# Kernel tuning notes

Measured on AMD Instinct MI355X. Metric: run time of the kernel, lower is better.

## Reference

```python
import jax, jax.numpy as jnp
import numpy as np

B, C, N = 4, 256, 4096
BN_EPS = 1e-5


def setup_inputs() -> dict:
    key = jax.random.key(0)
    ks = jax.random.split(key, 8)
    Cq = C // 4
    return {
        "x": jax.random.normal(ks[0], (B, C, N), dtype=jnp.float32),
        # q_conv and k_conv share weights (self.q_conv.weight = self.k_conv.weight)
        "w_qk": jax.random.normal(ks[1], (Cq, C), dtype=jnp.float32) * 0.05,
        "w_v": jax.random.normal(ks[2], (C, C), dtype=jnp.float32) * 0.05,
        "b_v": jax.random.normal(ks[3], (C,), dtype=jnp.float32) * 0.05,
        # LBR: Conv1d(C,C,1) + BN1d (inference stats) + ReLU
        "w_lbr": jax.random.normal(ks[4], (C, C), dtype=jnp.float32) * 0.05,
        "b_lbr": jax.random.normal(ks[5], (C,), dtype=jnp.float32) * 0.05,
        "bn_gamma": jnp.ones((C,), dtype=jnp.float32),
        "bn_beta": jnp.zeros((C,), dtype=jnp.float32),
        "bn_mean": jax.random.normal(ks[6], (C,), dtype=jnp.float32) * 0.05,
        "bn_var": jax.random.uniform(ks[7], (C,), dtype=jnp.float32, minval=0.5, maxval=1.5),
    }


def reference(x, w_qk, w_v, b_v, w_lbr, b_lbr, bn_gamma, bn_beta, bn_mean, bn_var):
    # x: [B, C, N]
    chans = x.shape[1]
    # conv1x1 Q/K (shared weight, no bias), V (with bias)
    x_q = jnp.einsum('qc,bcn->bnq', w_qk, x)          # [B, N, C/4]
    x_k = jnp.einsum('qc,bcm->bqm', w_qk, x)          # [B, C/4, N]
    x_v = jnp.einsum('oc,bcn->bon', w_v, x) + b_v[None, :, None]  # [B, C, N]
    # energy: [B, N_query, N_key]
    energy = jnp.einsum('bnq,bqm->bnm', x_q, x_k)
    # 'SL' normalization: scale by C**-0.5, softmax over dim=-2 (query axis)
    energy = energy * (chans ** -0.5)
    attention = jax.nn.softmax(energy, axis=-2)        # [B, N, N]
    # x_r[b,c,m] = sum_n x_v[b,c,n] * attention[b,n,m]
    x_r = jnp.einsum('bcn,bnm->bcm', x_v, attention)   # [B, C, N]
    # offset residual
    x_r = x - x_r
    # LBR: conv1x1 -> BN (inference) -> ReLU
    h = jnp.einsum('oc,bcn->bon', w_lbr, x_r) + b_lbr[None, :, None]
    inv_std = jax.lax.rsqrt(bn_var + BN_EPS)
    h = (h - bn_mean[None, :, None]) * (inv_std * bn_gamma)[None, :, None] + bn_beta[None, :, None]
    h = jax.nn.relu(h)
    return x + h
```

## Files before the change

### kernel.cpp

```cpp
#include <hip/hip_runtime.h>
#include <hip/hip_bf16.h>
#include <stdint.h>
#include <math.h>

#define Bq 4
#define Cc 256
#define Nn 4096
#define CQ 64
#define QKSCALE 0.30028060219661246f

typedef short s16x4 __attribute__((ext_vector_type(4)));
typedef short s16x8 __attribute__((ext_vector_type(8)));
typedef unsigned int u32x4 __attribute__((ext_vector_type(4)));
typedef float f32x16 __attribute__((ext_vector_type(16)));

#define MFMA32(a,b,c) __builtin_amdgcn_mfma_f32_32x32x16_bf16((a),(b),(c),0,0,0)

static __device__ __forceinline__ unsigned short f2b(float f) {
  unsigned int u = __float_as_uint(f);
  u += 0x7FFFu + ((u >> 16) & 1u);
  return (unsigned short)(u >> 16);
}

static __device__ __forceinline__ unsigned short f2bh(float f) {
  __hip_bfloat16 h = __float2bfloat16(f);
  return __builtin_bit_cast(unsigned short, h);
}

static __device__ __forceinline__ float b2f(unsigned short u) {
  return __uint_as_float(((unsigned int)u) << 16);
}

static __device__ __forceinline__ float fexp2(float x) {
#if __has_builtin(__builtin_amdgcn_exp2f)
  return __builtin_amdgcn_exp2f(x);
#else
  return exp2f(x);
#endif
}

static __device__ __forceinline__ f32x16 fz16() {
  f32x16 z;
#pragma unroll
  for (int i = 0; i < 16; i++) z[i] = 0.0f;
  return z;
}

static __device__ __forceinline__ float sum16(f32x16 E) {
  return (((E[0] + E[1]) + (E[2] + E[3])) + ((E[4] + E[5]) + (E[6] + E[7]))) +
         (((E[8] + E[9]) + (E[10] + E[11])) + ((E[12] + E[13]) + (E[14] + E[15])));
}

__global__ __launch_bounds__(256) void k_prep(
    const float* __restrict__ wqk, const float* __restrict__ wv,
    const float* __restrict__ wlbr, const float* __restrict__ blbr,
    const float* __restrict__ gamma, const float* __restrict__ beta,
    const float* __restrict__ mean, const float* __restrict__ var,
    unsigned short* __restrict__ Wcat, float* __restrict__ sd,
    unsigned int* __restrict__ mxb) {
  int bx = blockIdx.x, t = threadIdx.x;
  if (bx < 576) {
    float v;
    if (bx < 64) v = wqk[bx * 256 + t] * QKSCALE;
    else if (bx < 320) v = wv[(bx - 64) * 256 + t];
    else v = wlbr[(bx - 320) * 256 + t];
    Wcat[bx * 256 + t] = f2b(v);
  } else {
    float s = gamma[t] * rsqrtf(var[t] + 1e-5f);
    sd[t] = s;
    sd[256 + t] = beta[t] + (blbr[t] - mean[t]) * s;
    if (t < 4) mxb[t] = 0u;
  }
}

__global__ __launch_bounds__(640) void k_proj(const float* __restrict__ x,
                                              const unsigned short* __restrict__ Wcat,
                                              const float* __restrict__ bv,
                                              unsigned short* __restrict__ qkT,
                                              unsigned short* __restrict__ Vf,
                                              unsigned short* __restrict__ xT) {
  __shared__ unsigned short xs[32 * 264];
  int bx = blockIdx.x;
  int b = bx >> 7;
  int ntile = bx & 127;
  int n0 = ntile * 32;
  int t = threadIdx.x;
  const float* xb = x + (size_t)b * Cc * Nn;
  for (int u = t; u < 1024; u += 640) {
    int c = u >> 2, j = (u & 3) * 8;
    const float* src = &xb[(size_t)c * Nn + n0 + j];
    float4 v0 = *(const float4*)src;
    float4 v1 = *(const float4*)(src + 4);
    xs[(j + 0) * 264 + c] = f2b(v0.x);
    xs[(j + 1) * 264 + c] = f2b(v0.y);
    xs[(j + 2) * 264 + c] = f2b(v0.z);
    xs[(j + 3) * 264 + c] = f2b(v0.w);
    xs[(j + 4) * 264 + c] = f2b(v1.x);
    xs[(j + 5) * 264 + c] = f2b(v1.y);
    xs[(j + 6) * 264 + c] = f2b(v1.z);
    xs[(j + 7) * 264 + c] = f2b(v1.w);
  }
  int w = t >> 6, a = t & 31, g = (t >> 5) & 1;
  bool isqk = (w >= 8);
  int row0 = isqk ? (w - 8) * 32 : 64 + w * 32;
  s16x8 wf[16];
#pragma unroll
  for (int kc = 0; kc < 16; kc++)
    wf[kc] = *(const s16x8*)&Wcat[(size_t)(row0 + a) * 256 + kc * 16 + 8 * g];
  __syncthreads();
  unsigned short* xTb = xT + ((size_t)b * Nn + n0) * Cc;
  for (int u = t; u < 1024; u += 640) {
    int row = u >> 5, ch = u & 31;
    *(s16x8*)&xTb[(size_t)row * Cc + ch * 8] = *(const s16x8*)&xs[row * 264 + ch * 8];
  }
  f32x16 acc = fz16();
#pragma unroll
  for (int kc = 0; kc < 16; kc++) {
    s16x8 xf = *(const s16x8*)&xs[a * 264 + kc * 16 + 8 * g];
    acc = MFMA32(xf, wf[kc], acc);
  }
  if (isqk) {
    unsigned short* dst = qkT + ((size_t)b * Nn + n0) * CQ;
    int q0 = row0;
#pragma unroll
    for (int r = 0; r < 16; r++) {
      int n = (r & 3) + 8 * (r >> 2) + 4 * g;
      dst[(size_t)n * CQ + q0 + a] = f2b(acc[r]);
    }
  } else {
    int c0 = row0 - 64;
    float bvv = bv[c0 + a];
    s16x8 vlo, vhi;
#pragma unroll
    for (int r = 0; r < 8; r++) {
      vlo[r] = (short)f2b(acc[r] + bvv);
      vhi[r] = (short)f2b(acc[8 + r] + bvv);
    }
    unsigned short* dstF =
        Vf + ((size_t)(b * 128 + ntile) * 4 + g) * 2048 + (size_t)(c0 + a) * 8;
    *(s16x8*)dstF = vlo;
    *(s16x8*)(dstF + 4096) = vhi;
  }
}

__global__ __launch_bounds__(256) void k_norm(const unsigned short* __restrict__ qkT,
                                              float* __restrict__ nrm,
                                              unsigned int* __restrict__ mxb) {
  int idx = blockIdx.x * 256 + threadIdx.x;
  const unsigned short* row = qkT + (size_t)idx * CQ;
  float s = 0.0f;
#pragma unroll
  for (int k = 0; k < 8; k++) {
    s16x8 v = *(const s16x8*)&row[k * 8];
#pragma unroll
    for (int j = 0; j < 8; j++) {
      float f = b2f((unsigned short)v[j]);
      s += f * f;
    }
  }
  float nr = sqrtf(s);
  nrm[idx] = nr;
  float m = nr;
#pragma unroll
  for (int off = 1; off < 64; off <<= 1) m = fmaxf(m, __shfl_xor(m, off, 64));
  __shared__ float wm[4];
  if ((threadIdx.x & 63) == 0) wm[threadIdx.x >> 6] = m;
  __syncthreads();
  if (threadIdx.x == 0) {
    float mm = fmaxf(fmaxf(wm[0], wm[1]), fmaxf(wm[2], wm[3]));
    atomicMax(mxb + (idx >> 12), __float_as_uint(mm));
  }
}

__global__ __launch_bounds__(512, 2) void k_attn(const unsigned short* __restrict__ qkT,
                                                 const unsigned short* __restrict__ Vf,
                                                 const float* __restrict__ nrm,
                                                 const unsigned int* __restrict__ mxb,
                                                 unsigned short* __restrict__ xT) {
  __shared__ __align__(16) float Pf[4 * 128 * 33];
  __shared__ float Ls[4 * 64];
  int bx = blockIdx.x;
  int id = ((bx & 7) << 5) | (bx >> 3);
  int b = id >> 6;
  int m0 = (id & 63) * 64;
  int t = threadIdx.x;
  int w = t >> 6, a = t & 31, g = (t >> 5) & 1;
  int cs = w >> 2, ns = w & 3;
  const unsigned short* qkTb = qkT + (size_t)b * Nn * CQ;
  s16x8 Bq0[4], Bq1[4];
#pragma unroll
  for (int kc = 0; kc < 4; kc++) {
    Bq0[kc] = *(const s16x8*)&qkTb[(size_t)(m0 + a) * CQ + kc * 16 + 8 * g];
    Bq1[kc] = *(const s16x8*)&qkTb[(size_t)(m0 + 32 + a) * CQ + kc * 16 + 8 * g];
  }
  float mxf = __uint_as_float(mxb[b]);
  float Mh0 = nrm[(size_t)b * Nn + m0 + a] * mxf + 0.01f;
  float Mh1 = nrm[(size_t)b * Nn + m0 + 32 + a] * mxf + 0.01f;
  const unsigned short* Vc = Vf + (size_t)b * 1048576 + (size_t)g * 2048 +
                             (size_t)(cs * 128 + a) * 8;
  f32x16 acc[8];
#pragma unroll
  for (int i = 0; i < 8; i++) acc[i] = fz16();
  float Lp0 = 0.0f, Lp1 = 0.0f;
  s16x8 qf[4];
#pragma unroll
  for (int kc = 0; kc < 4; kc++)
    qf[kc] = *(const s16x8*)&qkTb[(size_t)(ns * 32 + a) * CQ + kc * 16 + 8 * g];
#pragma unroll 1
  for (int nt = ns; nt < 128; nt += 4) {
    const unsigned short* Vt = Vc + (size_t)nt * 8192;
    f32x16 E0 = fz16(), E1 = fz16();
#pragma unroll
    for (int kc = 0; kc < 4; kc++) E0 = MFMA32(qf[kc], Bq0[kc], E0);
    s16x8 va0, va1, va2, va3;
    va0 = *(const s16x8*)&Vt[0];
    va1 = *(const s16x8*)&Vt[4096];
    va2 = *(const s16x8*)&Vt[256];
    va3 = *(const s16x8*)&Vt[4096 + 256];
#pragma unroll
    for (int kc = 0; kc < 4; kc++) E1 = MFMA32(qf[kc], Bq1[kc], E1);
    int ntn = (nt + 4) & 127;
#pragma unroll
    for (int kc = 0; kc < 4; kc++)
      qf[kc] = *(const s16x8*)&qkTb[(size_t)(ntn * 32 + a) * CQ + kc * 16 + 8 * g];
#pragma unroll
    for (int r = 0; r < 16; r++) E0[r] = fexp2(E0[r] - Mh0);
    Lp0 += sum16(E0);
    s16x8 p00, p01;
#pragma unroll
    for (int j = 0; j < 8; j++) {
      p00[j] = (short)f2bh(E0[j]);
      p01[j] = (short)f2bh(E0[8 + j]);
    }
#pragma unroll
    for (int r = 0; r < 16; r++) E1[r] = fexp2(E1[r] - Mh1);
    Lp1 += sum16(E1);
    s16x8 p10, p11;
#pragma unroll
    for (int j = 0; j < 8; j++) {
      p10[j] = (short)f2bh(E1[j]);
      p11[j] = (short)f2bh(E1[8 + j]);
    }
    acc[0] = MFMA32(p00, va0, acc[0]);
    acc[4] = MFMA32(p10, va0, acc[4]);
    acc[1] = MFMA32(p00, va2, acc[1]);
    acc[5] = MFMA32(p10, va2, acc[5]);
    acc[0] = MFMA32(p01, va1, acc[0]);
    acc[4] = MFMA32(p11, va1, acc[4]);
    acc[1] = MFMA32(p01, va3, acc[1]);
    acc[5] = MFMA32(p11, va3, acc[5]);
    s16x8 vb0, vb1, vb2, vb3;
    vb0 = *(const s16x8*)&Vt[512];
    vb1 = *(const s16x8*)&Vt[4096 + 512];
    vb2 = *(const s16x8*)&Vt[768];
    vb3 = *(const s16x8*)&Vt[4096 + 768];
    acc[2] = MFMA32(p00, vb0, acc[2]);
    acc[6] = MFMA32(p10, vb0, acc[6]);
    acc[3] = MFMA32(p00, vb2, acc[3]);
    acc[7] = MFMA32(p10, vb2, acc[7]);
    acc[2] = MFMA32(p01, vb1, acc[2]);
    acc[6] = MFMA32(p11, vb1, acc[6]);
    acc[3] = MFMA32(p01, vb3, acc[3]);
    acc[7] = MFMA32(p11, vb3, acc[7]);
  }
  float Lw0 = Lp0 + __shfl_xor(Lp0, 32, 64);
  float Lw1 = Lp1 + __shfl_xor(Lp1, 32, 64);
  if (cs == 0 && (t & 63) < 32) {
    Ls[ns * 64 + a] = Lw0;
    Ls[ns * 64 + 32 + a] = Lw1;
  }
  unsigned short* xTb = xT + ((size_t)b * Nn + m0) * Cc;
#pragma unroll
  for (int q = 0; q < 4; q++) {
    int qmt = q >> 1, qcs = q & 1;
    __syncthreads();
    if (cs == qcs) {
#pragma unroll
      for (int ct = 0; ct < 4; ct++) {
        float* dst = &Pf[(size_t)(ns * 128 + ct * 32 + a) * 33];
        f32x16 A = acc[qmt * 4 + ct];
#pragma unroll
        for (int r = 0; r < 16; r++) {
          int mrow = (r & 3) + 8 * (r >> 2) + 4 * g;
          dst[mrow] = A[r];
        }
      }
    }
    __syncthreads();
    int m = t & 31, c8 = t >> 5;
    float rL = 1.0f / (((Ls[qmt * 32 + m] + Ls[64 + qmt * 32 + m]) +
                        (Ls[128 + qmt * 32 + m] + Ls[192 + qmt * 32 + m])));
    unsigned short* xrow = &xTb[(size_t)(qmt * 32 + m) * Cc + qcs * 128 + c8 * 8];
    s16x8 xv = *(const s16x8*)xrow;
#pragma unroll
    for (int j = 0; j < 8; j++) {
      int cl = c8 * 8 + j;
      float s = ((Pf[(0 * 128 + cl) * 33 + m] + Pf[(1 * 128 + cl) * 33 + m]) +
                 (Pf[(2 * 128 + cl) * 33 + m] + Pf[(3 * 128 + cl) * 33 + m]));
      xv[j] = (short)f2b(b2f((unsigned short)xv[j]) - s * rL);
    }
    *(s16x8*)xrow = xv;
  }
}

__global__ __launch_bounds__(512) void k_lbr(const unsigned short* __restrict__ xrT,
                                             const unsigned short* __restrict__ Wcat,
                                             const float* __restrict__ sd,
                                             const float* __restrict__ x,
                                             float* __restrict__ out) {
  __shared__ unsigned short xs[32 * 264];
  __shared__ float sL[256], dL[256];
  int bx = blockIdx.x;
  int b = bx >> 7;
  int n0 = (bx & 127) * 32;
  int t = threadIdx.x;
  const unsigned short* src = xrT + ((size_t)b * Nn + n0) * Cc;
  for (int u = t; u < 1024; u += 512) {
    int row = u >> 5, ch = u & 31;
    *(s16x8*)&xs[row * 264 + ch * 8] = *(const s16x8*)&src[row * Cc + ch * 8];
  }
  if (t < 256) {
    sL[t] = sd[t];
    dL[t] = sd[256 + t];
  }
  int w = t >> 6, a = t & 31, g = (t >> 5) & 1;
  int o0 = w * 32;
  s16x8 wf[16];
#pragma unroll
  for (int kc = 0; kc < 16; kc++)
    wf[kc] = *(const s16x8*)&Wcat[(size_t)(320 + o0 + a) * 256 + kc * 16 + 8 * g];
  __syncthreads();
  f32x16 acc = fz16();
#pragma unroll
  for (int kc = 0; kc < 16; kc++) {
    s16x8 xf = *(const s16x8*)&xs[a * 264 + kc * 16 + 8 * g];
    acc = MFMA32(wf[kc], xf, acc);
  }
  const float* xb = x + (size_t)b * Cc * Nn;
  float* ob = out + (size_t)b * Cc * Nn;
#pragma unroll
  for (int r = 0; r < 16; r++) {
    int o = o0 + (r & 3) + 8 * (r >> 2) + 4 * g;
    float v = acc[r] * sL[o] + dL[o];
    v = fmaxf(v, 0.0f);
    ob[(size_t)o * Nn + n0 + a] = xb[(size_t)o * Nn + n0 + a] + v;
  }
}

extern "C" void kernel_launch(void* const* d_in, const int* in_sizes, int n_in,
                              void* d_out, int out_size, void* d_ws, size_t ws_size,
                              hipStream_t stream) {
  (void)in_sizes; (void)n_in; (void)out_size; (void)ws_size;
  const float* x = (const float*)d_in[0];
  const float* wqk = (const float*)d_in[1];
  const float* wv = (const float*)d_in[2];
  const float* bv = (const float*)d_in[3];
  const float* wlbr = (const float*)d_in[4];
  const float* blbr = (const float*)d_in[5];
  const float* gamma = (const float*)d_in[6];
  const float* beta = (const float*)d_in[7];
  const float* mean = (const float*)d_in[8];
  const float* var = (const float*)d_in[9];
  char* ws = (char*)d_ws;
  unsigned short* qkT = (unsigned short*)ws;
  unsigned short* Vf = (unsigned short*)(ws + 2097152);
  unsigned short* xT = (unsigned short*)(ws + 10485760);
  float* sd = (float*)(ws + 18874368);
  unsigned short* Wcat = (unsigned short*)(ws + 18876416);
  float* out = (float*)d_out;
  float* nrm = (float*)d_out;
  unsigned int* mxb = (unsigned int*)((char*)d_out + 131072);

  k_prep<<<dim3(577), dim3(256), 0, stream>>>(wqk, wv, wlbr, blbr, gamma, beta,
                                              mean, var, Wcat, sd, mxb);
  k_proj<<<dim3(512), dim3(640), 0, stream>>>(x, Wcat, bv, qkT, Vf, xT);
  k_norm<<<dim3(64), dim3(256), 0, stream>>>(qkT, nrm, mxb);
  k_attn<<<dim3(256), dim3(512), 0, stream>>>(qkT, Vf, nrm, mxb, xT );
  k_lbr<<<dim3(512), dim3(512), 0, stream>>>(xT , Wcat, sd, x, out);
}
```

Baseline: 101.0 us.

## Software-pipeline QK energy MFMAs one tile ahead of softmax and PV

Restructures the attention main loop so the energy MFMAs for the next key tile are computed while exp/bf16 conversion of the current tile runs, using double-buffered energy registers and a 2x manual unroll. This aims to overlap MFMA latency with VALU exp work and hide the dependency between QK and softmax. It increases register pressure (two extra f32x16 sets), which may reduce occupancy or cause spills.

```diff
diff --git a/kernel.cpp b/kernel.cpp
--- a/kernel.cpp
+++ b/kernel.cpp
@@ -202,67 +202,84 @@
 #pragma unroll
   for (int i = 0; i < 8; i++) acc[i] = fz16();
   float Lp0 = 0.0f, Lp1 = 0.0f;
-  s16x8 qf[4];
-#pragma unroll
-  for (int kc = 0; kc < 4; kc++)
-    qf[kc] = *(const s16x8*)&qkTb[(size_t)(ns * 32 + a) * CQ + kc * 16 + 8 * g];
+  f32x16 EA0, EA1, EB0, EB1;
+  {
+    const unsigned short* qp = &qkTb[(size_t)(ns * 32 + a) * CQ + 8 * g];
+    s16x8 q0 = *(const s16x8*)(qp + 0);
+    s16x8 q1 = *(const s16x8*)(qp + 16);
+    s16x8 q2 = *(const s16x8*)(qp + 32);
+    s16x8 q3 = *(const s16x8*)(qp + 48);
+    EA0 = fz16(); EA1 = fz16();
+    EA0 = MFMA32(q0, Bq0[0], EA0); EA1 = MFMA32(q0, Bq1[0], EA1);
+    EA0 = MFMA32(q1, Bq0[1], EA0); EA1 = MFMA32(q1, Bq1[1], EA1);
+    EA0 = MFMA32(q2, Bq0[2], EA0); EA1 = MFMA32(q2, Bq1[2], EA1);
+    EA0 = MFMA32(q3, Bq0[3], EA0); EA1 = MFMA32(q3, Bq1[3], EA1);
+  }
+#define BODY(Ec0, Ec1, En0, En1, NTCUR, NTNXT)                                 \
+  do {                                                                         \
+    const unsigned short* Vt = Vc + (size_t)(NTCUR) * 8192;                    \
+    const unsigned short* qp = &qkTb[(size_t)((NTNXT) * 32 + a) * CQ + 8 * g]; \
+    s16x8 qn0 = *(const s16x8*)(qp + 0);                                       \
+    s16x8 qn1 = *(const s16x8*)(qp + 16);                                      \
+    s16x8 qn2 = *(const s16x8*)(qp + 32);                                      \
+    s16x8 qn3 = *(const s16x8*)(qp + 48);                                      \
+    s16x8 va0 = *(const s16x8*)&Vt[0];                                         \
+    s16x8 va1 = *(const s16x8*)&Vt[4096];                                      \
+    s16x8 va2 = *(const s16x8*)&Vt[256];                                       \
+    s16x8 va3 = *(const s16x8*)&Vt[4096 + 256];                                \
+                    \
+    s16x8 p00, p01;                                                            \
+    _Pragma("unroll") for (int r = 0; r < 16; r++)                             \
+        Ec0[r] = fexp2(Ec0[r] - Mh0);                                          \
+    Lp0 += sum16(Ec0);                                                         \
+    _Pragma("unroll") for (int j = 0; j < 8; j++) {                            \
+      p00[j] = (short)f2bh(Ec0[j]);                                            \
+      p01[j] = (short)f2bh(Ec0[8 + j]);                                        \
+    }                                                                          \
+                                   \
+    En0 = fz16(); En1 = fz16();                                                \
+    En0 = MFMA32(qn0, Bq0[0], En0); En1 = MFMA32(qn0, Bq1[0], En1);            \
+    En0 = MFMA32(qn1, Bq0[1], En0); En1 = MFMA32(qn1, Bq1[1], En1);            \
+    En0 = MFMA32(qn2, Bq0[2], En0); En1 = MFMA32(qn2, Bq1[2], En1);            \
+    En0 = MFMA32(qn3, Bq0[3], En0); En1 = MFMA32(qn3, Bq1[3], En1);            \
+            \
+    s16x8 p10, p11;                                                            \
+    _Pragma("unroll") for (int r = 0; r < 16; r++)                             \
+        Ec1[r] = fexp2(Ec1[r] - Mh1);                                          \
+    Lp1 += sum16(Ec1);                                                         \
+    _Pragma("unroll") for (int j = 0; j < 8; j++) {                            \
+      p10[j] = (short)f2bh(Ec1[j]);                                            \
+      p11[j] = (short)f2bh(Ec1[8 + j]);                                        \
+    }                                                                          \
+                    \
+    s16x8 vb0 = *(const s16x8*)&Vt[512];                                       \
+    s16x8 vb1 = *(const s16x8*)&Vt[4096 + 512];                                \
+    s16x8 vb2 = *(const s16x8*)&Vt[768];                                       \
+    s16x8 vb3 = *(const s16x8*)&Vt[4096 + 768];                                \
+    acc[0] = MFMA32(p00, va0, acc[0]);                                         \
+    acc[4] = MFMA32(p10, va0, acc[4]);                                         \
+    acc[1] = MFMA32(p00, va2, acc[1]);                                         \
+    acc[5] = MFMA32(p10, va2, acc[5]);                                         \
+    acc[0] = MFMA32(p01, va1, acc[0]);                                         \
+    acc[4] = MFMA32(p11, va1, acc[4]);                                         \
+    acc[1] = MFMA32(p01, va3, acc[1]);                                         \
+    acc[5] = MFMA32(p11, va3, acc[5]);                                         \
+    acc[2] = MFMA32(p00, vb0, acc[2]);                                         \
+    acc[6] = MFMA32(p10, vb0, acc[6]);                                         \
+    acc[3] = MFMA32(p00, vb2, acc[3]);                                         \
+    acc[7] = MFMA32(p10, vb2, acc[7]);                                         \
+    acc[2] = MFMA32(p01, vb1, acc[2]);                                         \
+    acc[6] = MFMA32(p11, vb1, acc[6]);                                         \
+    acc[3] = MFMA32(p01, vb3, acc[3]);                                         \
+    acc[7] = MFMA32(p11, vb3, acc[7]);                                         \
+  } while (0)
 #pragma unroll 1
-  for (int nt = ns; nt < 128; nt += 4) {
-    const unsigned short* Vt = Vc + (size_t)nt * 8192;
-    f32x16 E0 = fz16(), E1 = fz16();
-#pragma unroll
-    for (int kc = 0; kc < 4; kc++) E0 = MFMA32(qf[kc], Bq0[kc], E0);
-    s16x8 va0, va1, va2, va3;
-    va0 = *(const s16x8*)&Vt[0];
-    va1 = *(const s16x8*)&Vt[4096];
-    va2 = *(const s16x8*)&Vt[256];
-    va3 = *(const s16x8*)&Vt[4096 + 256];
-#pragma unroll
-    for (int kc = 0; kc < 4; kc++) E1 = MFMA32(qf[kc], Bq1[kc], E1);
-    int ntn = (nt + 4) & 127;
-#pragma unroll
-    for (int kc = 0; kc < 4; kc++)
-      qf[kc] = *(const s16x8*)&qkTb[(size_t)(ntn * 32 + a) * CQ + kc * 16 + 8 * g];
-#pragma unroll
-    for (int r = 0; r < 16; r++) E0[r] = fexp2(E0[r] - Mh0);
-    Lp0 += sum16(E0);
-    s16x8 p00, p01;
-#pragma unroll
-    for (int j = 0; j < 8; j++) {
-      p00[j] = (short)f2bh(E0[j]);
-      p01[j] = (short)f2bh(E0[8 + j]);
-    }
-#pragma unroll
-    for (int r = 0; r < 16; r++) E1[r] = fexp2(E1[r] - Mh1);
-    Lp1 += sum16(E1);
-    s16x8 p10, p11;
-#pragma unroll
-    for (int j = 0; j < 8; j++) {
-      p10[j] = (short)f2bh(E1[j]);
-      p11[j] = (short)f2bh(E1[8 + j]);
-    }
-    acc[0] = MFMA32(p00, va0, acc[0]);
-    acc[4] = MFMA32(p10, va0, acc[4]);
-    acc[1] = MFMA32(p00, va2, acc[1]);
-    acc[5] = MFMA32(p10, va2, acc[5]);
-    acc[0] = MFMA32(p01, va1, acc[0]);
-    acc[4] = MFMA32(p11, va1, acc[4]);
-    acc[1] = MFMA32(p01, va3, acc[1]);
-    acc[5] = MFMA32(p11, va3, acc[5]);
-    s16x8 vb0, vb1, vb2, vb3;
-    vb0 = *(const s16x8*)&Vt[512];
-    vb1 = *(const s16x8*)&Vt[4096 + 512];
-    vb2 = *(const s16x8*)&Vt[768];
-    vb3 = *(const s16x8*)&Vt[4096 + 768];
-    acc[2] = MFMA32(p00, vb0, acc[2]);
-    acc[6] = MFMA32(p10, vb0, acc[6]);
-    acc[3] = MFMA32(p00, vb2, acc[3]);
-    acc[7] = MFMA32(p10, vb2, acc[7]);
-    acc[2] = MFMA32(p01, vb1, acc[2]);
-    acc[6] = MFMA32(p11, vb1, acc[6]);
-    acc[3] = MFMA32(p01, vb3, acc[3]);
-    acc[7] = MFMA32(p11, vb3, acc[7]);
-  }
+  for (int i = 0; i < 16; i++) {
+    int nt = ns + i * 8;
+    BODY(EA0, EA1, EB0, EB1, nt, nt + 4);
+    BODY(EB0, EB1, EA0, EA1, nt + 4, (nt + 8) & 127);
+  }
+#undef BODY
   float Lw0 = Lp0 + __shfl_xor(Lp0, 32, 64);
   float Lw1 = Lp1 + __shfl_xor(Lp1, 32, 64);
   if (cs == 0 && (t & 63) < 32) {
```

Measured after the change: 157.2 us. +55.8%, slower.

## Split attention warps by query column half instead of channel half

Applied to the files above, without the earlier changes.

Each of the 8 warps now owns one 32-column m-slice and all 256 V channels, instead of both m-slices and half the channels. Every warp therefore computes one energy tile and one exp pass per iteration rather than two, which removes the duplicated QK^T and exp work that was repeated across channel halves. In exchange each warp loads twice as many V fragments per iteration (16 instead of 8), raising global/L2 traffic and register pressure. The epilogue reduction is reindexed to match the new ownership.

```diff
diff --git a/kernel.cpp b/kernel.cpp
--- a/kernel.cpp
+++ b/kernel.cpp
@@ -185,100 +185,99 @@
   int m0 = (id & 63) * 64;
   int t = threadIdx.x;
   int w = t >> 6, a = t & 31, g = (t >> 5) & 1;
-  int cs = w >> 2, ns = w & 3;
+  int ns = w >> 1, ms = w & 1;
   const unsigned short* qkTb = qkT + (size_t)b * Nn * CQ;
-  s16x8 Bq0[4], Bq1[4];
-#pragma unroll
-  for (int kc = 0; kc < 4; kc++) {
-    Bq0[kc] = *(const s16x8*)&qkTb[(size_t)(m0 + a) * CQ + kc * 16 + 8 * g];
-    Bq1[kc] = *(const s16x8*)&qkTb[(size_t)(m0 + 32 + a) * CQ + kc * 16 + 8 * g];
-  }
+  s16x8 Bqm[4];
+#pragma unroll
+  for (int kc = 0; kc < 4; kc++)
+    Bqm[kc] = *(const s16x8*)&qkTb[(size_t)(m0 + ms * 32 + a) * CQ + kc * 16 + 8 * g];
   float mxf = __uint_as_float(mxb[b]);
-  float Mh0 = nrm[(size_t)b * Nn + m0 + a] * mxf + 0.01f;
-  float Mh1 = nrm[(size_t)b * Nn + m0 + 32 + a] * mxf + 0.01f;
+  float Mh = nrm[(size_t)b * Nn + m0 + ms * 32 + a] * mxf + 0.01f;
   const unsigned short* Vc = Vf + (size_t)b * 1048576 + (size_t)g * 2048 +
-                             (size_t)(cs * 128 + a) * 8;
+                             (size_t)a * 8;
   f32x16 acc[8];
 #pragma unroll
   for (int i = 0; i < 8; i++) acc[i] = fz16();
-  float Lp0 = 0.0f, Lp1 = 0.0f;
-  s16x8 qf[4];
-#pragma unroll
-  for (int kc = 0; kc < 4; kc++)
-    qf[kc] = *(const s16x8*)&qkTb[(size_t)(ns * 32 + a) * CQ + kc * 16 + 8 * g];
+  float Lp = 0.0f;
+  s16x8 qf0, qf1, qf2, qf3;
+  {
+    const unsigned short* qp = &qkTb[(size_t)(ns * 32 + a) * CQ + 8 * g];
+    qf0 = *(const s16x8*)(qp + 0);
+    qf1 = *(const s16x8*)(qp + 16);
+    qf2 = *(const s16x8*)(qp + 32);
+    qf3 = *(const s16x8*)(qp + 48);
+  }
 #pragma unroll 1
-  for (int nt = ns; nt < 128; nt += 4) {
-    const unsigned short* Vt = Vc + (size_t)nt * 8192;
-    f32x16 E0 = fz16(), E1 = fz16();
-#pragma unroll
-    for (int kc = 0; kc < 4; kc++) E0 = MFMA32(qf[kc], Bq0[kc], E0);
-    s16x8 va0, va1, va2, va3;
-    va0 = *(const s16x8*)&Vt[0];
-    va1 = *(const s16x8*)&Vt[4096];
-    va2 = *(const s16x8*)&Vt[256];
-    va3 = *(const s16x8*)&Vt[4096 + 256];
-#pragma unroll
-    for (int kc = 0; kc < 4; kc++) E1 = MFMA32(qf[kc], Bq1[kc], E1);
-    int ntn = (nt + 4) & 127;
-#pragma unroll
-    for (int kc = 0; kc < 4; kc++)
-      qf[kc] = *(const s16x8*)&qkTb[(size_t)(ntn * 32 + a) * CQ + kc * 16 + 8 * g];
-#pragma unroll
-    for (int r = 0; r < 16; r++) E0[r] = fexp2(E0[r] - Mh0);
-    Lp0 += sum16(E0);
-    s16x8 p00, p01;
+  for (int i = 0; i < 32; i++) {
+    int ntc = ns + 4 * i;
+    const unsigned short* Vt = Vc + (size_t)ntc * 8192;
+    s16x8 va00 = *(const s16x8*)&Vt[0 * 256];
+    s16x8 va01 = *(const s16x8*)&Vt[1 * 256];
+    s16x8 va02 = *(const s16x8*)&Vt[2 * 256];
+    s16x8 va03 = *(const s16x8*)&Vt[3 * 256];
+    s16x8 va10 = *(const s16x8*)&Vt[4096 + 0 * 256];
+    s16x8 va11 = *(const s16x8*)&Vt[4096 + 1 * 256];
+    s16x8 va12 = *(const s16x8*)&Vt[4096 + 2 * 256];
+    s16x8 va13 = *(const s16x8*)&Vt[4096 + 3 * 256];
+    f32x16 E = fz16();
+    E = MFMA32(qf0, Bqm[0], E);
+    E = MFMA32(qf1, Bqm[1], E);
+    E = MFMA32(qf2, Bqm[2], E);
+    E = MFMA32(qf3, Bqm[3], E);
+    s16x8 vb00 = *(const s16x8*)&Vt[4 * 256];
+    s16x8 vb01 = *(const s16x8*)&Vt[5 * 256];
+    s16x8 vb02 = *(const s16x8*)&Vt[6 * 256];
+    s16x8 vb03 = *(const s16x8*)&Vt[7 * 256];
+    s16x8 vb10 = *(const s16x8*)&Vt[4096 + 4 * 256];
+    s16x8 vb11 = *(const s16x8*)&Vt[4096 + 5 * 256];
+    s16x8 vb12 = *(const s16x8*)&Vt[4096 + 6 * 256];
+    s16x8 vb13 = *(const s16x8*)&Vt[4096 + 7 * 256];
+    {
+      int ntn = (ntc + 4) & 127;
+      const unsigned short* qn = &qkTb[(size_t)(ntn * 32 + a) * CQ + 8 * g];
+      qf0 = *(const s16x8*)(qn + 0);
+      qf1 = *(const s16x8*)(qn + 16);
+      qf2 = *(const s16x8*)(qn + 32);
+      qf3 = *(const s16x8*)(qn + 48);
+    }
+    s16x8 p0, p1;
+#pragma unroll
+    for (int r = 0; r < 16; r++) E[r] = fexp2(E[r] - Mh);
+    Lp += sum16(E);
 #pragma unroll
     for (int j = 0; j < 8; j++) {
-      p00[j] = (short)f2bh(E0[j]);
-      p01[j] = (short)f2bh(E0[8 + j]);
-    }
-#pragma unroll
-    for (int r = 0; r < 16; r++) E1[r] = fexp2(E1[r] - Mh1);
-    Lp1 += sum16(E1);
-    s16x8 p10, p11;
-#pragma unroll
-    for (int j = 0; j < 8; j++) {
-      p10[j] = (short)f2bh(E1[j]);
-      p11[j] = (short)f2bh(E1[8 + j]);
-    }
-    acc[0] = MFMA32(p00, va0, acc[0]);
-    acc[4] = MFMA32(p10, va0, acc[4]);
-    acc[1] = MFMA32(p00, va2, acc[1]);
-    acc[5] = MFMA32(p10, va2, acc[5]);
-    acc[0] = MFMA32(p01, va1, acc[0]);
-    acc[4] = MFMA32(p11, va1, acc[4]);
-    acc[1] = MFMA32(p01, va3, acc[1]);
-    acc[5] = MFMA32(p11, va3, acc[5]);
-    s16x8 vb0, vb1, vb2, vb3;
-    vb0 = *(const s16x8*)&Vt[512];
-    vb1 = *(const s16x8*)&Vt[4096 + 512];
-    vb2 = *(const s16x8*)&Vt[768];
-    vb3 = *(const s16x8*)&Vt[4096 + 768];
-    acc[2] = MFMA32(p00, vb0, acc[2]);
-    acc[6] = MFMA32(p10, vb0, acc[6]);
-    acc[3] = MFMA32(p00, vb2, acc[3]);
-    acc[7] = MFMA32(p10, vb2, acc[7]);
-    acc[2] = MFMA32(p01, vb1, acc[2]);
-    acc[6] = MFMA32(p11, vb1, acc[6]);
-    acc[3] = MFMA32(p01, vb3, acc[3]);
-    acc[7] = MFMA32(p11, vb3, acc[7]);
-  }
-  float Lw0 = Lp0 + __shfl_xor(Lp0, 32, 64);
-  float Lw1 = Lp1 + __shfl_xor(Lp1, 32, 64);
-  if (cs == 0 && (t & 63) < 32) {
-    Ls[ns * 64 + a] = Lw0;
-    Ls[ns * 64 + 32 + a] = Lw1;
-  }
+      p0[j] = (short)f2bh(E[j]);
+      p1[j] = (short)f2bh(E[8 + j]);
+    }
+    acc[0] = MFMA32(p0, va00, acc[0]);
+    acc[1] = MFMA32(p0, va01, acc[1]);
+    acc[2] = MFMA32(p0, va02, acc[2]);
+    acc[3] = MFMA32(p0, va03, acc[3]);
+    acc[0] = MFMA32(p1, va10, acc[0]);
+    acc[1] = MFMA32(p1, va11, acc[1]);
+    acc[2] = MFMA32(p1, va12, acc[2]);
+    acc[3] = MFMA32(p1, va13, acc[3]);
+    acc[4] = MFMA32(p0, vb00, acc[4]);
+    acc[5] = MFMA32(p0, vb01, acc[5]);
+    acc[6] = MFMA32(p0, vb02, acc[6]);
+    acc[7] = MFMA32(p0, vb03, acc[7]);
+    acc[4] = MFMA32(p1, vb10, acc[4]);
+    acc[5] = MFMA32(p1, vb11, acc[5]);
+    acc[6] = MFMA32(p1, vb12, acc[6]);
+    acc[7] = MFMA32(p1, vb13, acc[7]);
+  }
+  float Lw = Lp + __shfl_xor(Lp, 32, 64);
+  if ((t & 63) < 32) Ls[ns * 64 + ms * 32 + a] = Lw;
   unsigned short* xTb = xT + ((size_t)b * Nn + m0) * Cc;
 #pragma unroll
   for (int q = 0; q < 4; q++) {
-    int qmt = q >> 1, qcs = q & 1;
+    int qms = q >> 1, qh = q & 1;
     __syncthreads();
-    if (cs == qcs) {
+    if (ms == qms) {
 #pragma unroll
       for (int ct = 0; ct < 4; ct++) {
         float* dst = &Pf[(size_t)(ns * 128 + ct * 32 + a) * 33];
-        f32x16 A = acc[qmt * 4 + ct];
+        f32x16 A = acc[qh * 4 + ct];
 #pragma unroll
         for (int r = 0; r < 16; r++) {
           int mrow = (r & 3) + 8 * (r >> 2) + 4 * g;
@@ -288,9 +287,9 @@
     }
     __syncthreads();
     int m = t & 31, c8 = t >> 5;
-    float rL = 1.0f / (((Ls[qmt * 32 + m] + Ls[64 + qmt * 32 + m]) +
-                        (Ls[128 + qmt * 32 + m] + Ls[192 + qmt * 32 + m])));
-    unsigned short* xrow = &xTb[(size_t)(qmt * 32 + m) * Cc + qcs * 128 + c8 * 8];
+    float rL = 1.0f / (((Ls[qms * 32 + m] + Ls[64 + qms * 32 + m]) +
+                        (Ls[128 + qms * 32 + m] + Ls[192 + qms * 32 + m])));
+    unsigned short* xrow = &xTb[(size_t)(qms * 32 + m) * Cc + qh * 128 + c8 * 8];
     s16x8 xv = *(const s16x8*)xrow;
 #pragma unroll
     for (int j = 0; j < 8; j++) {
```

Result: slower. 118.9 us (+17.7%).

## Fuse LBR conv/BN/ReLU epilogue into attention kernel and drop atomic max

Applied to the files above, without the earlier changes.

Moves the LBR stage (1x1 conv, BN, ReLU, residual) into the tail of the attention kernel. The residual tile now stays in shared memory instead of being written back to the xT buffer and reloaded by a separate launch. The per-batch norm maximum is no longer built with an atomic in k_norm; each attention block recomputes it by reducing all 4096 norms of its batch, and nrm moves into the workspace. The trade-off is a much larger LDS footprint per block, which may limit blocks per CU, plus redundant max reductions across blocks.

```diff
diff --git a/kernel.cpp b/kernel.cpp
--- a/kernel.cpp
+++ b/kernel.cpp
@@ -56,8 +56,7 @@
     const float* __restrict__ wlbr, const float* __restrict__ blbr,
     const float* __restrict__ gamma, const float* __restrict__ beta,
     const float* __restrict__ mean, const float* __restrict__ var,
-    unsigned short* __restrict__ Wcat, float* __restrict__ sd,
-    unsigned int* __restrict__ mxb) {
+    unsigned short* __restrict__ Wcat, float* __restrict__ sd) {
   int bx = blockIdx.x, t = threadIdx.x;
   if (bx < 576) {
     float v;
@@ -69,7 +68,6 @@
     float s = gamma[t] * rsqrtf(var[t] + 1e-5f);
     sd[t] = s;
     sd[256 + t] = beta[t] + (blbr[t] - mean[t]) * s;
-    if (t < 4) mxb[t] = 0u;
   }
 }
 
@@ -144,8 +142,7 @@
 }
 
 __global__ __launch_bounds__(256) void k_norm(const unsigned short* __restrict__ qkT,
-                                              float* __restrict__ nrm,
-                                              unsigned int* __restrict__ mxb) {
+                                              float* __restrict__ nrm) {
   int idx = blockIdx.x * 256 + threadIdx.x;
   const unsigned short* row = qkT + (size_t)idx * CQ;
   float s = 0.0f;
@@ -158,27 +155,22 @@
       s += f * f;
     }
   }
-  float nr = sqrtf(s);
-  nrm[idx] = nr;
-  float m = nr;
-#pragma unroll
-  for (int off = 1; off < 64; off <<= 1) m = fmaxf(m, __shfl_xor(m, off, 64));
-  __shared__ float wm[4];
-  if ((threadIdx.x & 63) == 0) wm[threadIdx.x >> 6] = m;
-  __syncthreads();
-  if (threadIdx.x == 0) {
-    float mm = fmaxf(fmaxf(wm[0], wm[1]), fmaxf(wm[2], wm[3]));
-    atomicMax(mxb + (idx >> 12), __float_as_uint(mm));
-  }
+  nrm[idx] = sqrtf(s);
 }
 
 __global__ __launch_bounds__(512, 2) void k_attn(const unsigned short* __restrict__ qkT,
                                                  const unsigned short* __restrict__ Vf,
                                                  const float* __restrict__ nrm,
-                                                 const unsigned int* __restrict__ mxb,
-                                                 unsigned short* __restrict__ xT) {
+                                                 const unsigned short* __restrict__ Wcat,
+                                                 const float* __restrict__ sd,
+                                                 const unsigned short* __restrict__ xT,
+                                                 const float* __restrict__ x,
+                                                 float* __restrict__ out) {
   __shared__ __align__(16) float Pf[4 * 128 * 33];
   __shared__ float Ls[4 * 64];
+  __shared__ unsigned short xs2[64 * 266];
+  __shared__ float sdL[512];
+  __shared__ float wmx[8];
   int bx = blockIdx.x;
   int id = ((bx & 7) << 5) | (bx >> 3);
   int b = id >> 6;
@@ -187,15 +179,25 @@
   int w = t >> 6, a = t & 31, g = (t >> 5) & 1;
   int cs = w >> 2, ns = w & 3;
   const unsigned short* qkTb = qkT + (size_t)b * Nn * CQ;
+  sdL[t < 512 ? t : 0] = sd[t < 512 ? t : 0];
+  const float* nrmb = nrm + (size_t)b * Nn;
+  float lm = 0.0f;
+#pragma unroll
+  for (int i = 0; i < 8; i++) lm = fmaxf(lm, nrmb[t + i * 512]);
+#pragma unroll
+  for (int off = 1; off < 64; off <<= 1) lm = fmaxf(lm, __shfl_xor(lm, off, 64));
+  if ((t & 63) == 0) wmx[w] = lm;
+  __syncthreads();
+  float mxf = fmaxf(fmaxf(fmaxf(wmx[0], wmx[1]), fmaxf(wmx[2], wmx[3])),
+                    fmaxf(fmaxf(wmx[4], wmx[5]), fmaxf(wmx[6], wmx[7])));
   s16x8 Bq0[4], Bq1[4];
 #pragma unroll
   for (int kc = 0; kc < 4; kc++) {
     Bq0[kc] = *(const s16x8*)&qkTb[(size_t)(m0 + a) * CQ + kc * 16 + 8 * g];
     Bq1[kc] = *(const s16x8*)&qkTb[(size_t)(m0 + 32 + a) * CQ + kc * 16 + 8 * g];
   }
-  float mxf = __uint_as_float(mxb[b]);
-  float Mh0 = nrm[(size_t)b * Nn + m0 + a] * mxf + 0.01f;
-  float Mh1 = nrm[(size_t)b * Nn + m0 + 32 + a] * mxf + 0.01f;
+  float Mh0 = nrmb[m0 + a] * mxf + 0.01f;
+  float Mh1 = nrmb[m0 + 32 + a] * mxf + 0.01f;
   const unsigned short* Vc = Vf + (size_t)b * 1048576 + (size_t)g * 2048 +
                              (size_t)(cs * 128 + a) * 8;
   f32x16 acc[8];
@@ -269,7 +271,7 @@
     Ls[ns * 64 + a] = Lw0;
     Ls[ns * 64 + 32 + a] = Lw1;
   }
-  unsigned short* xTb = xT + ((size_t)b * Nn + m0) * Cc;
+  const unsigned short* xTb = xT + ((size_t)b * Nn + m0) * Cc;
 #pragma unroll
   for (int q = 0; q < 4; q++) {
     int qmt = q >> 1, qcs = q & 1;
@@ -290,7 +292,7 @@
     int m = t & 31, c8 = t >> 5;
     float rL = 1.0f / (((Ls[qmt * 32 + m] + Ls[64 + qmt * 32 + m]) +
                         (Ls[128 + qmt * 32 + m] + Ls[192 + qmt * 32 + m])));
-    unsigned short* xrow = &xTb[(size_t)(qmt * 32 + m) * Cc + qcs * 128 + c8 * 8];
+    const unsigned short* xrow = &xTb[(size_t)(qmt * 32 + m) * Cc + qcs * 128 + c8 * 8];
     s16x8 xv = *(const s16x8*)xrow;
 #pragma unroll
     for (int j = 0; j < 8; j++) {
@@ -299,51 +301,32 @@
                  (Pf[(2 * 128 + cl) * 33 + m] + Pf[(3 * 128 + cl) * 33 + m]));
       xv[j] = (short)f2b(b2f((unsigned short)xv[j]) - s * rL);
     }
-    *(s16x8*)xrow = xv;
-  }
-}
-
-__global__ __launch_bounds__(512) void k_lbr(const unsigned short* __restrict__ xrT,
-                                             const unsigned short* __restrict__ Wcat,
-                                             const float* __restrict__ sd,
-                                             const float* __restrict__ x,
-                                             float* __restrict__ out) {
-  __shared__ unsigned short xs[32 * 264];
-  __shared__ float sL[256], dL[256];
-  int bx = blockIdx.x;
-  int b = bx >> 7;
-  int n0 = (bx & 127) * 32;
-  int t = threadIdx.x;
-  const unsigned short* src = xrT + ((size_t)b * Nn + n0) * Cc;
-  for (int u = t; u < 1024; u += 512) {
-    int row = u >> 5, ch = u & 31;
-    *(s16x8*)&xs[row * 264 + ch * 8] = *(const s16x8*)&src[row * Cc + ch * 8];
-  }
-  if (t < 256) {
-    sL[t] = sd[t];
-    dL[t] = sd[256 + t];
-  }
-  int w = t >> 6, a = t & 31, g = (t >> 5) & 1;
+    *(s16x8*)&xs2[(size_t)(qmt * 32 + m) * 266 + qcs * 128 + c8 * 8] = xv;
+  }
+  __syncthreads();
   int o0 = w * 32;
   s16x8 wf[16];
 #pragma unroll
   for (int kc = 0; kc < 16; kc++)
     wf[kc] = *(const s16x8*)&Wcat[(size_t)(320 + o0 + a) * 256 + kc * 16 + 8 * g];
-  __syncthreads();
-  f32x16 acc = fz16();
-#pragma unroll
-  for (int kc = 0; kc < 16; kc++) {
-    s16x8 xf = *(const s16x8*)&xs[a * 264 + kc * 16 + 8 * g];
-    acc = MFMA32(wf[kc], xf, acc);
-  }
   const float* xb = x + (size_t)b * Cc * Nn;
   float* ob = out + (size_t)b * Cc * Nn;
 #pragma unroll
-  for (int r = 0; r < 16; r++) {
-    int o = o0 + (r & 3) + 8 * (r >> 2) + 4 * g;
-    float v = acc[r] * sL[o] + dL[o];
-    v = fmaxf(v, 0.0f);
-    ob[(size_t)o * Nn + n0 + a] = xb[(size_t)o * Nn + n0 + a] + v;
+  for (int nsub = 0; nsub < 2; nsub++) {
+    f32x16 ac2 = fz16();
+#pragma unroll
+    for (int kc = 0; kc < 16; kc++) {
+      s16x8 xf = *(const s16x8*)&xs2[(size_t)(nsub * 32 + a) * 266 + kc * 16 + 8 * g];
+      ac2 = MFMA32(wf[kc], xf, ac2);
+    }
+    int n = m0 + nsub * 32 + a;
+#pragma unroll
+    for (int r = 0; r < 16; r++) {
+      int o = o0 + (r & 3) + 8 * (r >> 2) + 4 * g;
+      float v = ac2[r] * sdL[o] + sdL[256 + o];
+      v = fmaxf(v, 0.0f);
+      ob[(size_t)o * Nn + n] = xb[(size_t)o * Nn + n] + v;
+    }
   }
 }
 
@@ -367,14 +350,12 @@
   unsigned short* xT = (unsigned short*)(ws + 10485760);
   float* sd = (float*)(ws + 18874368);
   unsigned short* Wcat = (unsigned short*)(ws + 18876416);
+  float* nrm = (float*)(ws + 18876416 + 64 * 512);
   float* out = (float*)d_out;
-  float* nrm = (float*)d_out;
-  unsigned int* mxb = (unsigned int*)((char*)d_out + 131072);
 
   k_prep<<<dim3(577), dim3(256), 0, stream>>>(wqk, wv, wlbr, blbr, gamma, beta,
-                                              mean, var, Wcat, sd, mxb);
+                                              mean, var, Wcat, sd);
   k_proj<<<dim3(512), dim3(640), 0, stream>>>(x, Wcat, bv, qkT, Vf, xT);
-  k_norm<<<dim3(64), dim3(256), 0, stream>>>(qkT, nrm, mxb);
-  k_attn<<<dim3(256), dim3(512), 0, stream>>>(qkT, Vf, nrm, mxb, xT );
-  k_lbr<<<dim3(512), dim3(512), 0, stream>>>(xT , Wcat, sd, x, out);
-}
+  k_norm<<<dim3(64), dim3(256), 0, stream>>>(qkT, nrm);
+  k_attn<<<dim3(256), dim3(512), 0, stream>>>(qkT, Vf, nrm, Wcat, sd, xT, x, out);
+}
```

New measurement: 95.75 us. 1.05x faster.
